# Optimization experiments

Hardware: AMD Instinct MI355X
Metric: run time of the kernel (lower is better)

The kernel has to match this reference:

```python
import jax, jax.numpy as jnp
import numpy as np

N, E = 40000, 640000
D, H, DK = 128, 8, 16   # out_dim, n_heads, d_k = D // H
T, R = 3, 4             # num node types, num relation types


def setup_inputs() -> dict:
    key = jax.random.key(0)
    ks = jax.random.split(key, 16)
    glorot = lambda k, shape, fan: jax.random.normal(k, shape, jnp.float32) * np.sqrt(2.0 / fan)
    inp = {
        'node_inp': jax.random.normal(ks[0], (N, D), jnp.float32),
        'node_type': jax.random.randint(ks[1], (N,), 0, T),
        'edge_index': jax.random.randint(ks[2], (2, E), 0, N),
        'edge_type': jax.random.randint(ks[3], (E,), 0, R),
        'node_position': jax.random.randint(ks[4], (N,), 0, N),
        # per-node-type Linear weights, stored [T, in, out] (y = x @ W + b)
        'Kw': glorot(ks[5], (T, D, D), 2 * D), 'Kb': jnp.zeros((T, D), jnp.float32),
        'Qw': glorot(ks[6], (T, D, D), 2 * D), 'Qb': jnp.zeros((T, D), jnp.float32),
        'Vw': glorot(ks[7], (T, D, D), 2 * D), 'Vb': jnp.zeros((T, D), jnp.float32),
        'Aw': glorot(ks[8], (T, D, D), 2 * D), 'Ab': jnp.zeros((T, D), jnp.float32),
        'relation_pri': jnp.ones((T, R, T, H), jnp.float32),
        'relation_att': glorot(ks[9], (R, H, DK, DK), 2 * DK),
        'relation_msg': glorot(ks[10], (R, H, DK, DK), 2 * DK),
        'relation_s2u': glorot(ks[11], (D, D), 2 * D),
        'skip': jnp.ones((T,), jnp.float32),
    }
    return inp


def reference(node_inp, node_type, edge_index, edge_type, node_position,
              Kw, Kb, Qw, Qb, Vw, Vb, Aw, Ab,
              relation_pri, relation_att, relation_msg, relation_s2u, skip):
    n = node_inp.shape[0]
    src, tgt = edge_index[0], edge_index[1]  # j (source), i (target)
    ar = jnp.arange(n)

    # per-type K/Q/V projections for every node: [T, N, D], then select own type
    k_all = jnp.einsum('nd,tdo->tno', node_inp, Kw) + Kb[:, None, :]
    q_all = jnp.einsum('nd,tdo->tno', node_inp, Qw) + Qb[:, None, :]
    v_all = jnp.einsum('nd,tdo->tno', node_inp, Vw) + Vb[:, None, :]
    k_node = k_all[node_type, ar]
    q_node = q_all[node_type, ar]
    v_node = v_all[node_type, ar]

    k_j = k_node[src].reshape(-1, H, DK)
    v_j = v_node[src].reshape(-1, H, DK)
    q_i = q_node[tgt].reshape(-1, H, DK)

    # per-relation attention / message transforms (select per edge relation)
    k_t = jnp.zeros_like(k_j)
    v_t = jnp.zeros_like(v_j)
    for r in range(R):
        sel = (edge_type == r)[:, None, None]
        k_t = jnp.where(sel, jnp.einsum('ehd,hdf->ehf', k_j, relation_att[r]), k_t)
        v_t = jnp.where(sel, jnp.einsum('ehd,hdf->ehf', v_j, relation_msg[r]), v_t)

    st, tt = node_type[src], node_type[tgt]
    pri = relation_pri[tt, edge_type, st]                       # [E, H]
    att_raw = (q_i * k_t).sum(-1) * pri / np.sqrt(DK)           # [E, H]

    # scatter-softmax over edges sharing the same target node
    m = jax.ops.segment_max(att_raw, tgt, num_segments=n)
    m = jnp.where(jnp.isfinite(m), m, 0.0)
    ex = jnp.exp(att_raw - m[tgt])
    den = jax.ops.segment_sum(ex, tgt, num_segments=n)
    att = ex / (den[tgt] + 1e-16)

    msg = (v_t * att[:, :, None]).reshape(-1, D)
    aggr = jax.ops.segment_sum(msg, tgt, num_segments=n)        # scatter-add

    # speaker information: edges with edge_type==0, message from target rep to source index
    sp_in = v_all[1][tgt]                                       # v_linears[1](node_inp[edge_index_i])
    sp_msg = sp_in @ relation_s2u                               # [E, D]
    drop_idx = jnp.where(edge_type == 0, src, n)                # out-of-range -> dropped
    speaker_info = jnp.zeros((n, D), node_inp.dtype).at[drop_idx].set(sp_msg, mode='drop')

    aggr = jax.nn.gelu(aggr + speaker_info, approximate=False)

    # target-specific aggregation with per-type learnable skip (dropout=eval identity)
    a_all = jnp.einsum('no,tof->tnf', aggr, Aw) + Ab[:, None, :]
    a_node = a_all[node_type, ar]
    alpha = jax.nn.sigmoid(skip)[node_type][:, None]
    return a_node * alpha + node_inp * (1.0 - alpha)
```

## Files before the change

kernel.cpp:

```cpp
#include <hip/hip_runtime.h>
#include <hip/hip_bf16.h>
#include <math.h>

#define ND 128
#define NH 8
#define DKK 16
#define NT 3
#define NR 4
#define NB 8
#define NMAT 12
#define SCB 4096

typedef unsigned short ushort_t;
typedef __bf16 bf16_t;
typedef bf16_t bf16x8 __attribute__((ext_vector_type(8)));
typedef float f32x4 __attribute__((ext_vector_type(4)));

__device__ __forceinline__ float bf2f(unsigned short u) {
    union { unsigned int i; float f; } v; v.i = ((unsigned int)u) << 16; return v.f;
}
__device__ __forceinline__ unsigned short f2bf(float f) {
    union { float f; unsigned int i; } v; v.f = f;
    unsigned int x = v.i;
    unsigned int lsb = (x >> 16) & 1u;
    x += 0x7fffu + lsb;
    return (unsigned short)(x >> 16);
}
__device__ __forceinline__ unsigned int pk2(float a, float b) {
    return (unsigned int)f2bf(a) | ((unsigned int)f2bf(b) << 16);
}
__device__ __forceinline__ void load_bf8(const ushort_t* p, float* o) {
    uint4 u = *reinterpret_cast<const uint4*>(p);
    o[0]=bf2f(u.x & 0xffff); o[1]=bf2f(u.x >> 16);
    o[2]=bf2f(u.y & 0xffff); o[3]=bf2f(u.y >> 16);
    o[4]=bf2f(u.z & 0xffff); o[5]=bf2f(u.z >> 16);
    o[6]=bf2f(u.w & 0xffff); o[7]=bf2f(u.w >> 16);
}
__device__ __forceinline__ void cvt8(uint4 u, float* o) {
    o[0]=bf2f(u.x & 0xffff); o[1]=bf2f(u.x >> 16);
    o[2]=bf2f(u.y & 0xffff); o[3]=bf2f(u.y >> 16);
    o[4]=bf2f(u.z & 0xffff); o[5]=bf2f(u.z >> 16);
    o[6]=bf2f(u.w & 0xffff); o[7]=bf2f(u.w >> 16);
}
__device__ __forceinline__ bf16x8 as_bf16x8(uint4 u) {
    union { uint4 u; bf16x8 v; } c; c.u = u; return c.v;
}


__global__ void k_zero(int n, int* offs, int* winner) {
    int i = blockIdx.x * 256 + threadIdx.x;
    if (i < n) { offs[i] = 0; winner[i] = -1; }
}

__global__ void k_count(int e, const int* src, const int* tgt, const int* etype,
                        int* offs, int* winner, int* rank) {
    int i = blockIdx.x * 256 + threadIdx.x;
    if (i < e) {
        rank[i] = atomicAdd(&offs[tgt[i]], 1);
        if (etype[i] == 0) atomicMax(&winner[src[i]], i);
    }
}


__global__ void k_scanA(int n, const int* offs, const int* ntype, int* bsum4) {
    __shared__ int red[256];
    __shared__ int tr[256][3];
    int b = blockIdx.x, tid = threadIdx.x;
    int base = b * SCB + tid * 16;
    int s = 0, c0 = 0, c1 = 0, c2 = 0;
    #pragma unroll
    for (int i = 0; i < 16; i++) {
        int idx = base + i;
        if (idx < n) {
            s += offs[idx];
            int t = ntype[idx];
            c0 += (t == 0); c1 += (t == 1); c2 += (t == 2);
        }
    }
    red[tid] = s; tr[tid][0] = c0; tr[tid][1] = c1; tr[tid][2] = c2;
    __syncthreads();
    for (int d = 128; d > 0; d >>= 1) {
        if (tid < d) {
            red[tid] += red[tid + d];
            tr[tid][0] += tr[tid + d][0];
            tr[tid][1] += tr[tid + d][1];
            tr[tid][2] += tr[tid + d][2];
        }
        __syncthreads();
    }
    if (tid == 0) {
        bsum4[b * 4]     = red[0];
        bsum4[b * 4 + 1] = tr[0][0];
        bsum4[b * 4 + 2] = tr[0][1];
        bsum4[b * 4 + 3] = tr[0][2];
    }
}

__global__ void k_scanB(int nb, const int* bsum4, int* boff4, int* tcnt, int* tstart) {
    if (threadIdx.x == 0) {
        int run = 0, r0 = 0, r1 = 0, r2 = 0;
        for (int b = 0; b < nb; b++) {
            boff4[b * 4]     = run;
            boff4[b * 4 + 1] = r0;
            boff4[b * 4 + 2] = r1;
            boff4[b * 4 + 3] = r2;
            run += bsum4[b * 4];
            r0  += bsum4[b * 4 + 1];
            r1  += bsum4[b * 4 + 2];
            r2  += bsum4[b * 4 + 3];
        }
        tcnt[0] = r0; tcnt[1] = r1; tcnt[2] = r2;
        tstart[0] = 0; tstart[1] = r0; tstart[2] = r0 + r1;
    }
}

__global__ void k_scanC(int n, int* offs, const int* ntype, const int* boff4,
                        const int* tstart, int* order) {
    __shared__ int red[256];
    __shared__ int tr[256][3];
    int b = blockIdx.x, tid = threadIdx.x;
    int base = b * SCB + tid * 16;
    int v[16]; signed char ty[16];
    int s = 0, c0 = 0, c1 = 0, c2 = 0;
    #pragma unroll
    for (int i = 0; i < 16; i++) {
        int idx = base + i;
        v[i] = (idx < n) ? offs[idx] : 0;
        s += v[i];
        int t = (idx < n) ? ntype[idx] : -1;
        ty[i] = (signed char)t;
        c0 += (t == 0); c1 += (t == 1); c2 += (t == 2);
    }
    red[tid] = s; tr[tid][0] = c0; tr[tid][1] = c1; tr[tid][2] = c2;
    __syncthreads();
    for (int d = 1; d < 256; d <<= 1) {
        int vv = (tid >= d) ? red[tid - d] : 0;
        int w0 = (tid >= d) ? tr[tid - d][0] : 0;
        int w1 = (tid >= d) ? tr[tid - d][1] : 0;
        int w2 = (tid >= d) ? tr[tid - d][2] : 0;
        __syncthreads();
        red[tid] += vv; tr[tid][0] += w0; tr[tid][1] += w1; tr[tid][2] += w2;
        __syncthreads();
    }
    int run = boff4[b * 4] + red[tid] - s;
    int p0 = tstart[0] + boff4[b * 4 + 1] + tr[tid][0] - c0;
    int p1 = tstart[1] + boff4[b * 4 + 2] + tr[tid][1] - c1;
    int p2 = tstart[2] + boff4[b * 4 + 3] + tr[tid][2] - c2;
    #pragma unroll
    for (int i = 0; i < 16; i++) {
        int idx = base + i;
        if (idx < n) {
            offs[idx] = run; run += v[i];
            int t = ty[i];
            if (t == 0)      order[p0++] = idx;
            else if (t == 1) order[p1++] = idx;
            else             order[p2++] = idx;
        }
    }
    if (base <= n && n < base + 16) offs[n] = run;
}

__global__ void k_scatter(int e, const int* src, const int* tgt, const int* etype,
                          const int* ntype, const int* offs, const int* rank,
                          int* eord, int mode) {
    int i = blockIdx.x * 256 + threadIdx.x;
    if (i < e) {
        int p = offs[tgt[i]] + rank[i];
        if (mode) {
            int s = src[i];
            eord[p] = (s * NR + etype[i]) | (ntype[s] << 28);
        } else {
            eord[p] = i;
        }
    }
}


__global__ void k_pack(const float* Qw, const float* Qb, const float* Kw, const float* Kb,
                       const float* Vw, const float* Vb, const float* Aw, const float* Ab,
                       const float* s2u, const float* r_att, const float* r_msg,
                       ushort_t* Wall, float* bcat) {
    int blk = blockIdx.x;
    int kb = blk & 3;
    int c = (blk >> 2) & 7;
    int tm = blk >> 5;
    int m = tm % NMAT, t = tm / NMAT;
    int lane = threadIdx.x;
    int nn = c * 16 + (lane & 15);
    int quad = lane >> 4;
    int k0 = kb * 32 + quad * 8;
    ushort_t* dst = Wall + (size_t)blk * 512 + lane * 8;

    if (m == 0 || m == 5 || m == 10 || m == 11) {
        const float* W; const float* B;
        if (m == 0)       { W = Qw + (size_t)t * ND * ND; B = Qb + t * ND; }
        else if (m == 5)  { W = Vw + (size_t)ND * ND;     B = Vb + ND; }
        else if (m == 10) { W = Aw + (size_t)t * ND * ND; B = Ab + t * ND; }
        else              { W = s2u;                      B = nullptr; }
        #pragma unroll
        for (int j = 0; j < 8; j++) dst[j] = f2bf(W[(size_t)(k0 + j) * ND + nn]);
        if (kb == 0 && quad == 0)
            bcat[(t * NMAT + m) * ND + nn] = B ? B[nn] : 0.f;
    } else {
        int r = (m <= 4) ? (m - 1) : (m - 6);
        const float* W0 = (m <= 4) ? Kw : Vw;
        const float* B0 = (m <= 4) ? Kb : Vb;
        const float* Wr = (m <= 4) ? r_att : r_msg;
        int h = c, f = lane & 15;
        float wcol[16];
        #pragma unroll
        for (int jj = 0; jj < 16; jj++)
            wcol[jj] = Wr[(((size_t)r * NH + h) * DKK + jj) * DKK + f];
        #pragma unroll
        for (int j = 0; j < 8; j++) {
            const float* row = W0 + ((size_t)t * ND + (k0 + j)) * ND + h * DKK;
            float s = 0.f;
            #pragma unroll
            for (int jj = 0; jj < 16; jj++) s += row[jj] * wcol[jj];
            dst[j] = f2bf(s);
        }
        if (kb == 0 && quad == 0) {
            const float* brow = B0 + t * ND + h * DKK;
            float sb = 0.f;
            #pragma unroll
            for (int jj = 0; jj < 16; jj++) sb += brow[jj] * wcol[jj];
            bcat[(t * NMAT + m) * ND + nn] = sb;
        }
    }
}

__global__ void __launch_bounds__(256) k_projm(
    int n, const float* x_in, const int* order,
    const int* tcnt, const int* tstart,
    const ushort_t* Wall, const float* bcat,
    int m0, int nm,
    ushort_t* out_qn, ushort_t* out_kt, ushort_t* out_v1, ushort_t* out_vt)
{
    __shared__ __align__(16) ushort_t xs[4096];
    __shared__ int nodes[32];
    int b = blockIdx.x;
    int nb0 = (tcnt[0] + 31) >> 5, nb1 = (tcnt[1] + 31) >> 5, nb2 = (tcnt[2] + 31) >> 5;
    int t, lb;
    if (b < nb0)                  { t = 0; lb = b; }
    else if (b < nb0 + nb1)       { t = 1; lb = b - nb0; }
    else if (b < nb0 + nb1 + nb2) { t = 2; lb = b - nb0 - nb1; }
    else return;
    int segoff = lb * 32;
    int cnt = min(32, tcnt[t] - segoff);
    int segbase = tstart[t] + segoff;
    int tid = threadIdx.x;
    if (tid < 32) nodes[tid] = (tid < cnt) ? order[segbase + tid] : -1;
    __syncthreads();
    {
        int row = tid >> 3;
        int d0 = (tid & 7) * 16;
        int rt = row >> 4, rl = row & 15;
        int kb = d0 >> 5, q0 = (d0 >> 3) & 3;
        uint4 c0, c1;
        if (row < cnt) {
            const float4* xp4 = (const float4*)(x_in + (size_t)nodes[row] * ND + d0);
            float4 a = xp4[0], b2 = xp4[1], c2 = xp4[2], d4 = xp4[3];
            c0.x = pk2(a.x, a.y);   c0.y = pk2(a.z, a.w);
            c0.z = pk2(b2.x, b2.y); c0.w = pk2(b2.z, b2.w);
            c1.x = pk2(c2.x, c2.y); c1.y = pk2(c2.z, c2.w);
            c1.z = pk2(d4.x, d4.y); c1.w = pk2(d4.z, d4.w);
        } else {
            c0.x = c0.y = c0.z = c0.w = 0u;
            c1 = c0;
        }
        *(uint4*)&xs[((rt * 4 + kb) * 64 + q0 * 16 + rl) * 8]       = c0;
        *(uint4*)&xs[((rt * 4 + kb) * 64 + (q0 + 1) * 16 + rl) * 8] = c1;
    }
    __syncthreads();

    int w = tid >> 6, lane = tid & 63;
    int rt = w & 1;
    bf16x8 afr[4];
    #pragma unroll
    for (int kb = 0; kb < 4; kb++)
        afr[kb] = as_bf16x8(*(const uint4*)&xs[((rt * 4 + kb) * 64 + lane) * 8]);
    int nct = nm * 8;
    for (int ct = (w >> 1); ct < nct; ct += 2) {
        int m = m0 + (ct >> 3), c = ct & 7;
        const uint4* bp = (const uint4*)(Wall + ((((size_t)t * NMAT + m) * 8 + c) * 4) * 512);
        f32x4 acc = {0.f, 0.f, 0.f, 0.f};
        #pragma unroll
        for (int kb = 0; kb < 4; kb++) {
            bf16x8 bfr = as_bf16x8(bp[kb * 64 + lane]);
            acc = __builtin_amdgcn_mfma_f32_16x16x32_bf16(afr[kb], bfr, acc, 0, 0, 0);
        }
        int col = c * 16 + (lane & 15);
        float bias = bcat[(t * NMAT + m) * ND + col];
        int rbase = rt * 16 + (lane >> 4) * 4;
        #pragma unroll
        for (int r = 0; r < 4; r++) {
            int grow = rbase + r;
            if (grow >= cnt) continue;
            int node = nodes[grow];
            ushort_t val = f2bf(acc[r] + bias);
            if (m == 0)       out_qn[(size_t)node * ND + col] = val;
            else if (m <= 4)  out_kt[((size_t)node * NR + (m - 1)) * ND + col] = val;
            else if (m == 5)  out_v1[(size_t)node * ND + col] = val;
            else              out_vt[((size_t)node * NR + (m - 6)) * ND + col] = val;
        }
    }
}

__global__ void __launch_bounds__(256) k_projall(
    int n, const float* x_in, const int* order,
    const int* tcnt, const int* tstart,
    const ushort_t* Wall, const float* bcat,
    ushort_t* out_qn, ushort_t* out_kt, ushort_t* out_v1, ushort_t* out_vt)
{
    __shared__ __align__(16) ushort_t xs[4096];
    __shared__ int nodes[32];
    int b = blockIdx.x;
    int nb0 = (tcnt[0] + 31) >> 5, nb1 = (tcnt[1] + 31) >> 5, nb2 = (tcnt[2] + 31) >> 5;
    int t, lb;
    if (b < nb0)                  { t = 0; lb = b; }
    else if (b < nb0 + nb1)       { t = 1; lb = b - nb0; }
    else if (b < nb0 + nb1 + nb2) { t = 2; lb = b - nb0 - nb1; }
    else return;
    int segoff = lb * 32;
    int cnt = min(32, tcnt[t] - segoff);
    int segbase = tstart[t] + segoff;
    int tid = threadIdx.x;
    if (tid < 32) nodes[tid] = (tid < cnt) ? order[segbase + tid] : -1;
    __syncthreads();
    {
        int row = tid >> 3;
        int d0 = (tid & 7) * 16;
        int rt = row >> 4, rl = row & 15;
        int kb = d0 >> 5, q0 = (d0 >> 3) & 3;
        uint4 c0, c1;
        if (row < cnt) {
            const float4* xp4 = (const float4*)(x_in + (size_t)nodes[row] * ND + d0);
            float4 a = xp4[0], b2 = xp4[1], c2 = xp4[2], d4 = xp4[3];
            c0.x = pk2(a.x, a.y);   c0.y = pk2(a.z, a.w);
            c0.z = pk2(b2.x, b2.y); c0.w = pk2(b2.z, b2.w);
            c1.x = pk2(c2.x, c2.y); c1.y = pk2(c2.z, c2.w);
            c1.z = pk2(d4.x, d4.y); c1.w = pk2(d4.z, d4.w);
        } else {
            c0.x = c0.y = c0.z = c0.w = 0u;
            c1 = c0;
        }
        *(uint4*)&xs[((rt * 4 + kb) * 64 + q0 * 16 + rl) * 8]       = c0;
        *(uint4*)&xs[((rt * 4 + kb) * 64 + (q0 + 1) * 16 + rl) * 8] = c1;
    }
    __syncthreads();

    int w = tid >> 6, lane = tid & 63;
    int rt = w & 1;
    bf16x8 afr[4];
    #pragma unroll
    for (int kb = 0; kb < 4; kb++)
        afr[kb] = as_bf16x8(*(const uint4*)&xs[((rt * 4 + kb) * 64 + lane) * 8]);
    for (int ct = (w >> 1); ct < 80; ct += 2) {
        int m = ct >> 3, c = ct & 7;
        const uint4* bp = (const uint4*)(Wall + ((((size_t)t * NMAT + m) * 8 + c) * 4) * 512);
        f32x4 acc = {0.f, 0.f, 0.f, 0.f};
        #pragma unroll
        for (int kb = 0; kb < 4; kb++) {
            bf16x8 bfr = as_bf16x8(bp[kb * 64 + lane]);
            acc = __builtin_amdgcn_mfma_f32_16x16x32_bf16(afr[kb], bfr, acc, 0, 0, 0);
        }
        int col = c * 16 + (lane & 15);
        float bias = bcat[(t * NMAT + m) * ND + col];
        int rbase = rt * 16 + (lane >> 4) * 4;
        #pragma unroll
        for (int r = 0; r < 4; r++) {
            int grow = rbase + r;
            if (grow >= cnt) continue;
            int node = nodes[grow];
            ushort_t val = f2bf(acc[r] + bias);
            if (m == 0)       out_qn[(size_t)node * ND + col] = val;
            else if (m <= 4)  out_kt[((size_t)node * NR + (m - 1)) * ND + col] = val;
            else if (m == 5)  out_v1[(size_t)node * ND + col] = val;
            else              out_vt[((size_t)node * NR + (m - 6)) * ND + col] = val;
        }
    }
}

__global__ void __launch_bounds__(256) k_flash(
    int n, const int* off, const int* srp, const int* ntype,
    const ushort_t* qn, const ushort_t* kt, const ushort_t* vt,
    const float* r_pri, float* aggr)
{
    int wv = threadIdx.x >> 6, lane = threadIdx.x & 63;
    int i = blockIdx.x * 4 + wv;
    if (i >= n) return;
    int h = lane & 7, slot = lane >> 3;
    int hA = lane >> 3;
    int tt = ntype[i];
    float qf[16];
    load_bf8(qn + (size_t)i * ND + h * DKK, qf);
    load_bf8(qn + (size_t)i * ND + h * DKK + 8, qf + 8);
    const float* prib = r_pri + (size_t)(tt * NR * NT) * NH + h;
    int d0 = off[i], d1 = off[i + 1];
    float m = -3.0e38f, den = 0.f;
    float acc0 = 0.f, acc1 = 0.f;
    int sp_c = 0; bool live_c = false;
    uint4 ka_c, kb_c;
    ka_c.x = ka_c.y = ka_c.z = ka_c.w = 0u; kb_c = ka_c;
    if (d0 < d1) {
        int p = d0 + slot;
        live_c = (p < d1);
        sp_c = live_c ? srp[p] : 0;
        const uint4* kp = (const uint4*)(kt + (size_t)(sp_c & 0x0fffffff) * ND + h * DKK);
        ka_c = kp[0]; kb_c = kp[1];
    }
    for (int p0 = d0; p0 < d1; p0 += 8) {
        int np0 = p0 + 8;
        int sp_n = 0; bool live_n = false;
        uint4 ka_n, kb_n;
        ka_n.x = ka_n.y = ka_n.z = ka_n.w = 0u; kb_n = ka_n;
        if (np0 < d1) {
            int p = np0 + slot;
            live_n = (p < d1);
            sp_n = live_n ? srp[p] : 0;
            const uint4* kp = (const uint4*)(kt + (size_t)(sp_n & 0x0fffffff) * ND + h * DKK);
            ka_n = kp[0]; kb_n = kp[1];
        }
        int sr = sp_c & 0x0fffffff;
        int st = ((unsigned int)sp_c) >> 28;
        int r = sr & (NR - 1);
        float kf[16];
        cvt8(ka_c, kf); cvt8(kb_c, kf + 8);
        float a = 0.f;
        #pragma unroll
        for (int f = 0; f < 16; f++) a += qf[f] * kf[f];
        float pri = prib[(r * NT + st) * NH];
        float logit = fminf(fmaxf(a * pri * 0.25f, -1.0e4f), 1.0e4f);
        if (!live_c) logit = -3.0e38f;
        int nlive = min(d1 - p0, 8);
        unsigned int u[8];
        #pragma unroll
        for (int s = 0; s < 8; s++) {
            int srb = __shfl(sr, s * 8 + hA, 64);
            u[s] = (s < nlive) ? *reinterpret_cast<const unsigned int*>(
                        vt + (size_t)srb * ND + lane * 2) : 0u;
        }
        float cm = logit;
        #pragma unroll
        for (int d = 8; d < 64; d <<= 1) cm = fmaxf(cm, __shfl_xor(cm, d, 64));
        float mnew = fmaxf(m, cm);
        float w = live_c ? expf(logit - mnew) : 0.f;
        float ws = w;
        #pragma unroll
        for (int d = 8; d < 64; d <<= 1) ws += __shfl_xor(ws, d, 64);
        float scale = expf(m - mnew);
        den = den * scale + ws;
        m = mnew;
        float scaleA = __shfl(scale, hA, 64);
        acc0 *= scaleA; acc1 *= scaleA;
        #pragma unroll
        for (int s = 0; s < 8; s++) {
            if (s < nlive) {
                float wb = __shfl(w, s * 8 + hA, 64);
                acc0 += wb * bf2f(u[s] & 0xffff);
                acc1 += wb * bf2f(u[s] >> 16);
            }
        }
        sp_c = sp_n; live_c = live_n; ka_c = ka_n; kb_c = kb_n;
    }
    float denA = __shfl(den, hA, 64);
    float inv = 1.f / (denA + 1e-16f);
    float2 o; o.x = acc0 * inv; o.y = acc1 * inv;
    *reinterpret_cast<float2*>(aggr + (size_t)i * ND + lane * 2) = o;
}

__global__ void __launch_bounds__(256) k_sfinal(
    int n, const float* x_in, const int* order, const int* tcnt, const int* tstart,
    const int* winner, const int* tgt, const ushort_t* v1b,
    const ushort_t* Wall, const float* bcat, const float* skip,
    const float* aggr, float* out)
{
    __shared__ __align__(16) float xf[32 * 132];
    __shared__ __align__(16) ushort_t xs[4096];
    __shared__ int nodes[32];
    __shared__ int wsrc[32];
    int b = blockIdx.x;
    int nb0 = (tcnt[0] + 31) >> 5, nb1 = (tcnt[1] + 31) >> 5, nb2 = (tcnt[2] + 31) >> 5;
    int t, lb;
    if (b < nb0)                  { t = 0; lb = b; }
    else if (b < nb0 + nb1)       { t = 1; lb = b - nb0; }
    else if (b < nb0 + nb1 + nb2) { t = 2; lb = b - nb0 - nb1; }
    else return;
    int segoff = lb * 32;
    int cnt = min(32, tcnt[t] - segoff);
    int segbase = tstart[t] + segoff;
    int tid = threadIdx.x;
    if (tid < 32) {
        int nd = (tid < cnt) ? order[segbase + tid] : -1;
        nodes[tid] = nd;
        int wi = (nd >= 0) ? winner[nd] : -1;
        wsrc[tid] = (wi >= 0) ? tgt[wi] : -1;
    }
    __syncthreads();
    {
        int row = tid >> 3;
        int d0 = (tid & 7) * 16;
        int rt = row >> 4, rl = row & 15;
        int kb = d0 >> 5, q0 = (d0 >> 3) & 3;
        uint4 c0, c1;
        int s = (row < cnt) ? wsrc[row] : -1;
        if (s >= 0) {
            const uint4* vp = (const uint4*)(v1b + (size_t)s * ND + d0);
            c0 = vp[0]; c1 = vp[1];
        } else { c0.x = c0.y = c0.z = c0.w = 0u; c1 = c0; }
        *(uint4*)&xs[((rt * 4 + kb) * 64 + q0 * 16 + rl) * 8]       = c0;
        *(uint4*)&xs[((rt * 4 + kb) * 64 + (q0 + 1) * 16 + rl) * 8] = c1;
    }
    __syncthreads();
    int w = tid >> 6, lane = tid & 63;
    int rt = w & 1;
    {
        bf16x8 afr[4];
        #pragma unroll
        for (int kb = 0; kb < 4; kb++)
            afr[kb] = as_bf16x8(*(const uint4*)&xs[((rt * 4 + kb) * 64 + lane) * 8]);
        for (int ct = (w >> 1); ct < 8; ct += 2) {
            const uint4* bp = (const uint4*)(Wall + (((size_t)11 * 8 + ct) * 4) * 512);
            f32x4 acc = {0.f, 0.f, 0.f, 0.f};
            #pragma unroll
            for (int kb = 0; kb < 4; kb++) {
                bf16x8 bfr = as_bf16x8(bp[kb * 64 + lane]);
                acc = __builtin_amdgcn_mfma_f32_16x16x32_bf16(afr[kb], bfr, acc, 0, 0, 0);
            }
            int col = ct * 16 + (lane & 15);
            int rbase = rt * 16 + (lane >> 4) * 4;
            #pragma unroll
            for (int r = 0; r < 4; r++) {
                int grow = rbase + r;
                if (grow >= cnt) continue;
                int node = nodes[grow];
                float g = aggr[(size_t)node * ND + col] + acc[r];
                g = 0.5f * g * (1.f + erff(g * 0.70710678118f));
                xf[grow * 132 + col] = g;
            }
        }
    }
    __syncthreads();
    {
        int row = tid >> 3;
        int d0 = (tid & 7) * 16;
        int rt2 = row >> 4, rl = row & 15;
        int kb = d0 >> 5, q0 = (d0 >> 3) & 3;
        uint4 c0, c1;
        if (row < cnt) {
            const float4* xp4 = (const float4*)(xf + row * 132 + d0);
            float4 a = xp4[0], b2 = xp4[1], c2 = xp4[2], d4 = xp4[3];
            c0.x = pk2(a.x, a.y);   c0.y = pk2(a.z, a.w);
            c0.z = pk2(b2.x, b2.y); c0.w = pk2(b2.z, b2.w);
            c1.x = pk2(c2.x, c2.y); c1.y = pk2(c2.z, c2.w);
            c1.z = pk2(d4.x, d4.y); c1.w = pk2(d4.z, d4.w);
        } else {
            c0.x = c0.y = c0.z = c0.w = 0u;
            c1 = c0;
        }
        *(uint4*)&xs[((rt2 * 4 + kb) * 64 + q0 * 16 + rl) * 8]       = c0;
        *(uint4*)&xs[((rt2 * 4 + kb) * 64 + (q0 + 1) * 16 + rl) * 8] = c1;
    }
    __syncthreads();
    float alpha = 1.f / (1.f + expf(-skip[t]));
    {
        bf16x8 afr[4];
        #pragma unroll
        for (int kb = 0; kb < 4; kb++)
            afr[kb] = as_bf16x8(*(const uint4*)&xs[((rt * 4 + kb) * 64 + lane) * 8]);
        for (int ct = (w >> 1); ct < 8; ct += 2) {
            const uint4* bp = (const uint4*)(Wall + ((((size_t)t * NMAT + 10) * 8 + ct) * 4) * 512);
            f32x4 acc = {0.f, 0.f, 0.f, 0.f};
            #pragma unroll
            for (int kb = 0; kb < 4; kb++) {
                bf16x8 bfr = as_bf16x8(bp[kb * 64 + lane]);
                acc = __builtin_amdgcn_mfma_f32_16x16x32_bf16(afr[kb], bfr, acc, 0, 0, 0);
            }
            int col = ct * 16 + (lane & 15);
            float bias = bcat[(t * NMAT + 10) * ND + col];
            int rbase = rt * 16 + (lane >> 4) * 4;
            #pragma unroll
            for (int r = 0; r < 4; r++) {
                int grow = rbase + r;
                if (grow >= cnt) continue;
                int node = nodes[grow];
                float xin = x_in[(size_t)node * ND + col];
                out[(size_t)node * ND + col] = (acc[r] + bias) * alpha + xin * (1.f - alpha);
            }
        }
    }
}

__global__ void __launch_bounds__(256) k_attmd(
    int n, const int* off, const int* srp, const int* ntype,
    const ushort_t* qn, const ushort_t* kt, const float* r_pri,
    float* atts, ushort_t* mb, float* db)
{
    int wv = threadIdx.x >> 6, lane = threadIdx.x & 63;
    int i = blockIdx.x * 4 + wv;
    if (i >= n) return;
    int h = lane & 7, slot = lane >> 3;
    int tt = ntype[i];
    float qf[16];
    load_bf8(qn + (size_t)i * ND + h * DKK, qf);
    load_bf8(qn + (size_t)i * ND + h * DKK + 8, qf + 8);
    const float* prib = r_pri + (size_t)(tt * NR * NT) * NH + h;
    int d0 = off[i], d1 = off[i + 1];
    float m = -3.0e38f, den = 0.f;
    #pragma unroll 2
    for (int p0 = d0; p0 < d1; p0 += 8) {
        int p = p0 + slot;
        bool live = (p < d1);
        int sp = live ? srp[p] : 0;
        int sr = sp & 0x0fffffff;
        int st = ((unsigned int)sp) >> 28;
        int r = sr & (NR - 1);
        float kf[16];
        const ushort_t* kp = kt + (size_t)sr * ND + h * DKK;
        load_bf8(kp, kf);
        load_bf8(kp + 8, kf + 8);
        float a = 0.f;
        #pragma unroll
        for (int f = 0; f < 16; f++) a += qf[f] * kf[f];
        float pri = prib[(r * NT + st) * NH];
        float logit = fminf(fmaxf(a * pri * 0.25f, -1.0e4f), 1.0e4f);
        if (live) {
            atts[(size_t)p * NH + h] = logit;
            float mnew = fmaxf(m, logit);
            den = den * expf(m - mnew) + expf(logit - mnew);
            m = mnew;
        }
    }
    #pragma unroll
    for (int d = 8; d < 64; d <<= 1) {
        float mo = __shfl_xor(m, d, 64);
        float dn = __shfl_xor(den, d, 64);
        float mnew = fmaxf(m, mo);
        den = den * expf(m - mnew) + dn * expf(mo - mnew);
        m = mnew;
    }
    if (slot == 0) {
        ushort_t mh = (d1 > d0) ? f2bf(m) : (ushort_t)0;
        float dfin = (d1 > d0) ? den * expf(m - bf2f(mh)) : 0.f;
        mb[i * NH + h] = mh;
        db[i * NH + h] = dfin;
    }
}

__global__ void __launch_bounds__(256) k_aggr_fast(
    int n, const int* off, const int* srp, const ushort_t* vt, const float* atts,
    const ushort_t* mb, const float* db, float* aggr)
{
    int wv = threadIdx.x >> 6, lane = threadIdx.x & 63;
    int i = blockIdx.x * 4 + wv;
    if (i >= n) return;
    int h = lane >> 3;
    float mref = bf2f(mb[i * NH + h]);
    float inv = 1.f / (db[i * NH + h] + 1e-16f);
    int d0 = off[i], d1 = off[i + 1];
    float acc0 = 0.f, acc1 = 0.f;
    #pragma unroll 4
    for (int p = d0; p < d1; p++) {
        int sr = srp[p] & 0x0fffffff;
        float w = expf(atts[(size_t)p * NH + h] - mref) * inv;
        unsigned int u = *reinterpret_cast<const unsigned int*>(
            vt + (size_t)sr * ND + lane * 2);
        acc0 += w * bf2f(u & 0xffff);
        acc1 += w * bf2f(u >> 16);
    }
    float2 o; o.x = acc0; o.y = acc1;
    *reinterpret_cast<float2*>(aggr + (size_t)i * ND + lane * 2) = o;
}


__global__ void k_proj(int n, const float* x_in, const int* ntype, const int* order,
                       const float* Kw, const float* Kb,
                       const float* Qw, const float* Qb,
                       const float* Vw, const float* Vb,
                       ushort_t* kn, ushort_t* qn, ushort_t* vn, ushort_t* v1) {
    __shared__ float xs[NB][ND];
    __shared__ int nodes[NB];
    __shared__ int types[NB];
    int tid = threadIdx.x;
    int base = blockIdx.x * NB;
    int cnt = min(NB, n - base);
    if (tid < cnt) { int nd = order[base + tid]; nodes[tid] = nd; types[tid] = ntype[nd]; }
    __syncthreads();
    for (int j = 0; j < cnt; j++) xs[j][tid] = x_in[(size_t)nodes[j] * ND + tid];
    __syncthreads();
    bool uni = (types[0] == types[cnt - 1]);
    for (int m = 0; m < 4; m++) {
        const float *W, *B; ushort_t* out; int forced_t = -1;
        if (m == 0)      { W = Kw; B = Kb; out = kn; }
        else if (m == 1) { W = Qw; B = Qb; out = qn; }
        else if (m == 2) { W = Vw; B = Vb; out = vn; }
        else             { W = Vw; B = Vb; out = v1; forced_t = 1; }
        if (uni || forced_t >= 0) {
            int t = (forced_t >= 0) ? forced_t : types[0];
            float bias = B[t * ND + tid];
            float acc[NB];
            #pragma unroll
            for (int j = 0; j < NB; j++) acc[j] = bias;
            const float* Wp = W + (size_t)t * ND * ND + tid;
            for (int d = 0; d < ND; d++) {
                float w = Wp[(size_t)d * ND];
                #pragma unroll
                for (int j = 0; j < NB; j++) acc[j] += xs[j][d] * w;
            }
            for (int j = 0; j < cnt; j++) out[(size_t)nodes[j] * ND + tid] = f2bf(acc[j]);
        } else {
            for (int j = 0; j < cnt; j++) {
                int t = types[j];
                float acc = B[t * ND + tid];
                const float* Wp = W + (size_t)t * ND * ND + tid;
                for (int d = 0; d < ND; d++) acc += xs[j][d] * Wp[(size_t)d * ND];
                out[(size_t)nodes[j] * ND + tid] = f2bf(acc);
            }
        }
    }
}

__global__ void k_att(int e, const int* src, const int* tgt, const int* etype, const int* ntype,
                      const ushort_t* kn, const ushort_t* qn,
                      const float* r_att, const float* r_pri, float* att) {
    int id = blockIdx.x * 256 + threadIdx.x;
    if (id >= e * NH) return;
    int ee = id >> 3, h = id & 7;
    int s = src[ee], t = tgt[ee], r = etype[ee];
    float kf[16], qf[16];
    load_bf8(kn + (size_t)s * ND + h * DKK, kf);
    load_bf8(kn + (size_t)s * ND + h * DKK + 8, kf + 8);
    load_bf8(qn + (size_t)t * ND + h * DKK, qf);
    load_bf8(qn + (size_t)t * ND + h * DKK + 8, qf + 8);
    const float* W = r_att + (size_t)(r * NH + h) * DKK * DKK;
    float kt[16];
    #pragma unroll
    for (int f = 0; f < 16; f++) kt[f] = 0.f;
    #pragma unroll 4
    for (int d = 0; d < 16; d++) {
        float kd = kf[d];
        #pragma unroll
        for (int f = 0; f < 16; f++) kt[f] += kd * W[d * 16 + f];
    }
    float a = 0.f;
    #pragma unroll
    for (int f = 0; f < 16; f++) a += qf[f] * kt[f];
    int tt = ntype[t], st = ntype[s];
    float pri = r_pri[((tt * NR + r) * NT + st) * NH + h];
    float logit = a * pri * 0.25f;
    logit = fminf(fmaxf(logit, -1.0e4f), 1.0e4f);
    att[(size_t)ee * NH + h] = logit;
}

__global__ void k_mden(int n, const int* off, const int* sorted,
                       const float* att, ushort_t* mb, float* db) {
    int id = blockIdx.x * 256 + threadIdx.x;
    if (id >= n * NH) return;
    int i = id >> 3, h = id & 7;
    int d0 = off[i], d1 = off[i + 1];
    float m = -3.0e38f;
    for (int p = d0; p < d1; p++) m = fmaxf(m, att[(size_t)sorted[p] * NH + h]);
    ushort_t mh = (d1 > d0) ? f2bf(m) : (ushort_t)0;
    float mref = bf2f(mh);
    float den = 0.f;
    for (int p = d0; p < d1; p++) den += expf(att[(size_t)sorted[p] * NH + h] - mref);
    mb[id] = mh;
    db[id] = den;
}

__global__ void k_norm(int e, const int* tgt, const ushort_t* mb, const float* db, float* att) {
    int id = blockIdx.x * 256 + threadIdx.x;
    if (id >= e * NH) return;
    int ee = id >> 3, h = id & 7;
    int t = tgt[ee];
    float w = expf(att[id] - bf2f(mb[t * NH + h])) / (db[t * NH + h] + 1e-16f);
    att[id] = w;
}

__global__ void k_aggr(int n, const int* off, const int* sorted, const int* src, const int* etype,
                       const ushort_t* vn, const float* r_msg, const float* att, float* aggr) {
    int wv = threadIdx.x >> 6, lane = threadIdx.x & 63;
    int i = blockIdx.x * 4 + wv;
    if (i >= n) return;
    int h = lane >> 3, f0 = (lane & 7) * 2;
    int d0 = off[i], d1 = off[i + 1];
    float acc0 = 0.f, acc1 = 0.f;
    for (int p = d0; p < d1; p++) {
        int ee = sorted[p];
        int s = src[ee], r = etype[ee];
        float w = att[(size_t)ee * NH + h];
        float vj[16];
        load_bf8(vn + (size_t)s * ND + h * DKK, vj);
        load_bf8(vn + (size_t)s * ND + h * DKK + 8, vj + 8);
        const float* Wm = r_msg + (size_t)(r * NH + h) * DKK * DKK + f0;
        float a0 = 0.f, a1 = 0.f;
        #pragma unroll
        for (int d = 0; d < 16; d++) {
            a0 += vj[d] * Wm[d * 16];
            a1 += vj[d] * Wm[d * 16 + 1];
        }
        acc0 += w * a0; acc1 += w * a1;
    }
    aggr[(size_t)i * ND + h * DKK + f0]     = acc0;
    aggr[(size_t)i * ND + h * DKK + f0 + 1] = acc1;
}

__global__ void k_spk(int n, const int* winner, const int* tgt, const ushort_t* v1,
                      const float* s2u, float* aggr) {
    __shared__ float xs[NB][ND];
    __shared__ int wn[NB];
    int tid = threadIdx.x;
    int base = blockIdx.x * NB;
    int cnt = min(NB, n - base);
    if (tid < cnt) wn[tid] = winner[base + tid];
    __syncthreads();
    for (int j = 0; j < cnt; j++) {
        int w = wn[j];
        xs[j][tid] = (w >= 0) ? bf2f(v1[(size_t)tgt[w] * ND + tid]) : 0.f;
    }
    __syncthreads();
    float acc[NB];
    #pragma unroll
    for (int j = 0; j < NB; j++) acc[j] = 0.f;
    const float* Wp = s2u + tid;
    for (int d = 0; d < ND; d++) {
        float w = Wp[(size_t)d * ND];
        #pragma unroll
        for (int j = 0; j < NB; j++) acc[j] += xs[j][d] * w;
    }
    for (int j = 0; j < cnt; j++) {
        size_t idx = (size_t)(base + j) * ND + tid;
        float g = aggr[idx] + acc[j];
        g = 0.5f * g * (1.f + erff(g * 0.70710678118f));
        aggr[idx] = g;
    }
}

__global__ void k_final(int n, const float* x_in, const int* ntype, const int* order,
                        const float* Aw, const float* Ab, const float* skip,
                        const float* aggr, float* out) {
    __shared__ float xs[NB][ND];
    __shared__ int nodes[NB];
    __shared__ int types[NB];
    int tid = threadIdx.x;
    int base = blockIdx.x * NB;
    int cnt = min(NB, n - base);
    if (tid < cnt) { int nd = order[base + tid]; nodes[tid] = nd; types[tid] = ntype[nd]; }
    __syncthreads();
    for (int j = 0; j < cnt; j++) xs[j][tid] = aggr[(size_t)nodes[j] * ND + tid];
    __syncthreads();
    bool uni = (types[0] == types[cnt - 1]);
    if (uni) {
        int t = types[0];
        float bias = Ab[t * ND + tid];
        float acc[NB];
        #pragma unroll
        for (int j = 0; j < NB; j++) acc[j] = bias;
        const float* Wp = Aw + (size_t)t * ND * ND + tid;
        for (int d = 0; d < ND; d++) {
            float w = Wp[(size_t)d * ND];
            #pragma unroll
            for (int j = 0; j < NB; j++) acc[j] += xs[j][d] * w;
        }
        float alpha = 1.f / (1.f + expf(-skip[t]));
        for (int j = 0; j < cnt; j++) {
            float xin = x_in[(size_t)nodes[j] * ND + tid];
            out[(size_t)nodes[j] * ND + tid] = acc[j] * alpha + xin * (1.f - alpha);
        }
    } else {
        for (int j = 0; j < cnt; j++) {
            int t = types[j];
            float acc = Ab[t * ND + tid];
            const float* Wp = Aw + (size_t)t * ND * ND + tid;
            for (int d = 0; d < ND; d++) acc += xs[j][d] * Wp[(size_t)d * ND];
            float alpha = 1.f / (1.f + expf(-skip[t]));
            float xin = x_in[(size_t)nodes[j] * ND + tid];
            out[(size_t)nodes[j] * ND + tid] = acc * alpha + xin * (1.f - alpha);
        }
    }
}

extern "C" void kernel_launch(void* const* d_in, const int* in_sizes, int n_in,
                              void* d_out, int out_size, void* d_ws, size_t ws_size,
                              hipStream_t stream) {
    const float* node_inp = (const float*)d_in[0];
    const int* node_type  = (const int*)d_in[1];
    const int* edge_index = (const int*)d_in[2];
    const int* edge_type  = (const int*)d_in[3];
    const float* Kw = (const float*)d_in[5];
    const float* Kb = (const float*)d_in[6];
    const float* Qw = (const float*)d_in[7];
    const float* Qb = (const float*)d_in[8];
    const float* Vw = (const float*)d_in[9];
    const float* Vb = (const float*)d_in[10];
    const float* Aw = (const float*)d_in[11];
    const float* Ab = (const float*)d_in[12];
    const float* r_pri = (const float*)d_in[13];
    const float* r_att = (const float*)d_in[14];
    const float* r_msg = (const float*)d_in[15];
    const float* s2u   = (const float*)d_in[16];
    const float* skip  = (const float*)d_in[17];

    int n = in_sizes[1];
    int e = in_sizes[3];
    const int* srcp = edge_index;
    const int* tgtp = edge_index + e;

    char* wsp = (char*)d_ws;
    size_t woff = 0;
    auto alloc = [&](size_t b) { void* p = wsp + woff; woff += (b + 255) & ~(size_t)255; return p; };

    int* offs     = (int*)alloc((size_t)(n + 1) * 4);
    int* winner   = (int*)alloc((size_t)n * 4);
    int* order    = (int*)alloc((size_t)n * 4);
    int* tcnt     = (int*)alloc(16);
    int* tstart   = (int*)alloc(16);
    int* bsum4    = (int*)alloc(4096);
    int* boff4    = (int*)alloc(4096);
    int* eord     = (int*)alloc((size_t)e * 4);
    ushort_t* mb  = (ushort_t*)alloc((size_t)n * NH * 2);
    float* db     = (float*)alloc((size_t)n * NH * 4);
    ushort_t* v1b = (ushort_t*)alloc((size_t)n * ND * 2);
    float* att    = (float*)alloc((size_t)e * NH * 4);
    size_t commonEnd = woff;

    int* rank = (int*)att;

    woff = commonEnd;
    ushort_t* WallB = (ushort_t*)alloc((size_t)NT * NMAT * 8 * 4 * 512 * 2);
    float* bcatB    = (float*)alloc((size_t)NT * NMAT * ND * 4);
    char* F         = (char*)alloc((size_t)n * 1536);
    size_t fastEnd = woff;

    woff = commonEnd;
    ushort_t* WallA = (ushort_t*)alloc((size_t)NT * NMAT * 8 * 4 * 512 * 2);
    float* bcatA    = (float*)alloc((size_t)NT * NMAT * ND * 4);
    ushort_t* qnA   = (ushort_t*)alloc((size_t)n * ND * 2);
    ushort_t* ktA   = (ushort_t*)alloc((size_t)n * NR * ND * 2);
    ushort_t* vtA   = (ushort_t*)alloc((size_t)n * NR * ND * 2);
    size_t tierAEnd = woff;
    float* aggrA = (float*)att;

    int gn = (n + 255) / 256;
    int ge = (e + 255) / 256;
    int nbscan = n / SCB + 1;
    int gproj = (n + 31) / 32 + NT;

    int tierA = (ws_size >= tierAEnd) && ((size_t)e * NH >= (size_t)n * ND);
    int fast  = (ws_size >= fastEnd);

    k_zero<<<gn, 256, 0, stream>>>(n, offs, winner);
    k_count<<<ge, 256, 0, stream>>>(e, srcp, tgtp, edge_type, offs, winner, rank);
    k_scanA<<<nbscan, 256, 0, stream>>>(n, offs, node_type, bsum4);
    k_scanB<<<1, 64, 0, stream>>>(nbscan, bsum4, boff4, tcnt, tstart);
    k_scanC<<<nbscan, 256, 0, stream>>>(n, offs, node_type, boff4, tstart, order);
    k_scatter<<<ge, 256, 0, stream>>>(e, srcp, tgtp, edge_type, node_type, offs, rank,
                                      eord, (tierA || fast) ? 1 : 0);

    if (tierA) {
        k_pack<<<NT * NMAT * 8 * 4, 64, 0, stream>>>(Qw, Qb, Kw, Kb, Vw, Vb, Aw, Ab,
                                                     s2u, r_att, r_msg, WallA, bcatA);
        k_projall<<<gproj, 256, 0, stream>>>(n, node_inp, order, tcnt, tstart, WallA, bcatA,
                                             qnA, ktA, v1b, vtA);
        k_flash<<<(n + 3) / 4, 256, 0, stream>>>(n, offs, eord, node_type,
                                                 qnA, ktA, vtA, r_pri, aggrA);
        k_sfinal<<<gproj, 256, 0, stream>>>(n, node_inp, order, tcnt, tstart,
                                            winner, tgtp, v1b, WallA, bcatA, skip,
                                            aggrA, (float*)d_out);
    } else if (fast) {
        ushort_t* qn  = (ushort_t*)F;
        ushort_t* kt  = (ushort_t*)(F + (size_t)n * 256);
        ushort_t* vt  = (ushort_t*)F;
        float* aggr   = (float*)(F + (size_t)n * 1024);

        k_pack<<<NT * NMAT * 8 * 4, 64, 0, stream>>>(Qw, Qb, Kw, Kb, Vw, Vb, Aw, Ab,
                                                     s2u, r_att, r_msg, WallB, bcatB);
        k_projm<<<gproj, 256, 0, stream>>>(n, node_inp, order, tcnt, tstart, WallB, bcatB,
                                           0, 6, qn, kt, v1b, (ushort_t*)nullptr);
        k_attmd<<<(n + 3) / 4, 256, 0, stream>>>(n, offs, eord, node_type,
                                                 qn, kt, r_pri, att, mb, db);
        k_projm<<<gproj, 256, 0, stream>>>(n, node_inp, order, tcnt, tstart, WallB, bcatB,
                                           6, 4, (ushort_t*)nullptr, (ushort_t*)nullptr,
                                           (ushort_t*)nullptr, vt);
        k_aggr_fast<<<(n + 3) / 4, 256, 0, stream>>>(n, offs, eord, vt, att, mb, db, aggr);
        k_sfinal<<<gproj, 256, 0, stream>>>(n, node_inp, order, tcnt, tstart,
                                            winner, tgtp, v1b, WallB, bcatB, skip,
                                            aggr, (float*)d_out);
    } else {
        woff = commonEnd;
        ushort_t* vn  = (ushort_t*)alloc((size_t)n * ND * 2);
        char* regA    = (char*)alloc((size_t)n * ND * 2 * 2);
        ushort_t* kn  = (ushort_t*)regA;
        ushort_t* qn  = (ushort_t*)(regA + (size_t)n * ND * 2);
        float* aggr   = (float*)regA;

        k_proj<<<(n + NB - 1) / NB, 128, 0, stream>>>(n, node_inp, node_type, order,
                                                      Kw, Kb, Qw, Qb, Vw, Vb, kn, qn, vn, v1b);
        k_att<<<(e * NH + 255) / 256, 256, 0, stream>>>(e, srcp, tgtp, edge_type, node_type,
                                                        kn, qn, r_att, r_pri, att);
        k_mden<<<(n * NH + 255) / 256, 256, 0, stream>>>(n, offs, eord, att, mb, db);
        k_norm<<<(e * NH + 255) / 256, 256, 0, stream>>>(e, tgtp, mb, db, att);
        k_aggr<<<(n + 3) / 4, 256, 0, stream>>>(n, offs, eord, srcp, edge_type, vn, r_msg, att, aggr);
        k_spk<<<(n + NB - 1) / NB, 128, 0, stream>>>(n, winner, tgtp, v1b, s2u, aggr);
        k_final<<<(n + NB - 1) / NB, 128, 0, stream>>>(n, node_inp, node_type, order,
                                                       Aw, Ab, skip, aggr, (float*)d_out);
    }
}
```

Baseline: 312.7 us.

## Apply relation message transform after aggregation instead of precomputing per-relation V

Rather than projecting V through each of the four relation_msg matrices per node (n×4×D output), the projection now writes a single per-type V, and the flash kernel keeps four per-relation accumulators. It then applies the relation_msg 16x16 transform once per node at the end using shuffles. This cuts projection MFMA work and the per-node V storage and gather traffic by a factor of four. In exchange the flash kernel gets more registers, a data-dependent branch per edge, and a 64-step shuffle-multiply epilogue that reads weights from global memory.

```diff
diff --git a/kernel.cpp b/kernel.cpp
--- a/kernel.cpp
+++ b/kernel.cpp
@@ -8,7 +8,7 @@
 #define NT 3
 #define NR 4
 #define NB 8
-#define NMAT 12
+#define NMAT 13
 #define SCB 4096
 
 typedef unsigned short ushort_t;
@@ -191,11 +191,12 @@
     int k0 = kb * 32 + quad * 8;
     ushort_t* dst = Wall + (size_t)blk * 512 + lane * 8;
 
-    if (m == 0 || m == 5 || m == 10 || m == 11) {
+    if (m == 0 || m == 5 || m == 10 || m == 11 || m == 12) {
         const float* W; const float* B;
         if (m == 0)       { W = Qw + (size_t)t * ND * ND; B = Qb + t * ND; }
         else if (m == 5)  { W = Vw + (size_t)ND * ND;     B = Vb + ND; }
         else if (m == 10) { W = Aw + (size_t)t * ND * ND; B = Ab + t * ND; }
+        else if (m == 12) { W = Vw + (size_t)t * ND * ND; B = Vb + t * ND; }
         else              { W = s2u;                      B = nullptr; }
         #pragma unroll
         for (int j = 0; j < 8; j++) dst[j] = f2bf(W[(size_t)(k0 + j) * ND + nn]);
@@ -310,7 +311,7 @@
     int n, const float* x_in, const int* order,
     const int* tcnt, const int* tstart,
     const ushort_t* Wall, const float* bcat,
-    ushort_t* out_qn, ushort_t* out_kt, ushort_t* out_v1, ushort_t* out_vt)
+    ushort_t* out_qn, ushort_t* out_kt, ushort_t* out_v1, ushort_t* out_vn)
 {
     __shared__ __align__(16) ushort_t xs[4096];
     __shared__ int nodes[32];
@@ -355,8 +356,9 @@
     #pragma unroll
     for (int kb = 0; kb < 4; kb++)
         afr[kb] = as_bf16x8(*(const uint4*)&xs[((rt * 4 + kb) * 64 + lane) * 8]);
-    for (int ct = (w >> 1); ct < 80; ct += 2) {
-        int m = ct >> 3, c = ct & 7;
+    for (int ci = (w >> 1); ci < 56; ci += 2) {
+        int m = (ci < 48) ? (ci >> 3) : 12;
+        int c = ci & 7;
         const uint4* bp = (const uint4*)(Wall + ((((size_t)t * NMAT + m) * 8 + c) * 4) * 512);
         f32x4 acc = {0.f, 0.f, 0.f, 0.f};
         #pragma unroll
@@ -376,15 +378,15 @@
             if (m == 0)       out_qn[(size_t)node * ND + col] = val;
             else if (m <= 4)  out_kt[((size_t)node * NR + (m - 1)) * ND + col] = val;
             else if (m == 5)  out_v1[(size_t)node * ND + col] = val;
-            else              out_vt[((size_t)node * NR + (m - 6)) * ND + col] = val;
+            else              out_vn[(size_t)node * ND + col] = val;
         }
     }
 }
 
 __global__ void __launch_bounds__(256) k_flash(
     int n, const int* off, const int* srp, const int* ntype,
-    const ushort_t* qn, const ushort_t* kt, const ushort_t* vt,
-    const float* r_pri, float* aggr)
+    const ushort_t* qn, const ushort_t* kt, const ushort_t* vn,
+    const float* r_pri, const float* r_msg, float* aggr)
 {
     int wv = threadIdx.x >> 6, lane = threadIdx.x & 63;
     int i = blockIdx.x * 4 + wv;
@@ -398,7 +400,8 @@
     const float* prib = r_pri + (size_t)(tt * NR * NT) * NH + h;
     int d0 = off[i], d1 = off[i + 1];
     float m = -3.0e38f, den = 0.f;
-    float acc0 = 0.f, acc1 = 0.f;
+    float a00 = 0.f, a01 = 0.f, a02 = 0.f, a03 = 0.f;
+    float a10 = 0.f, a11 = 0.f, a12 = 0.f, a13 = 0.f;
     int sp_c = 0; bool live_c = false;
     uint4 ka_c, kb_c;
     ka_c.x = ka_c.y = ka_c.z = ka_c.w = 0u; kb_c = ka_c;
@@ -434,11 +437,13 @@
         if (!live_c) logit = -3.0e38f;
         int nlive = min(d1 - p0, 8);
         unsigned int u[8];
+        int rbv[8];
         #pragma unroll
         for (int s = 0; s < 8; s++) {
             int srb = __shfl(sr, s * 8 + hA, 64);
+            rbv[s] = srb & (NR - 1);
             u[s] = (s < nlive) ? *reinterpret_cast<const unsigned int*>(
-                        vt + (size_t)srb * ND + lane * 2) : 0u;
+                        vn + (size_t)(srb >> 2) * ND + lane * 2) : 0u;
         }
         float cm = logit;
         #pragma unroll
@@ -452,20 +457,41 @@
         den = den * scale + ws;
         m = mnew;
         float scaleA = __shfl(scale, hA, 64);
-        acc0 *= scaleA; acc1 *= scaleA;
+        a00 *= scaleA; a01 *= scaleA; a02 *= scaleA; a03 *= scaleA;
+        a10 *= scaleA; a11 *= scaleA; a12 *= scaleA; a13 *= scaleA;
         #pragma unroll
         for (int s = 0; s < 8; s++) {
             if (s < nlive) {
                 float wb = __shfl(w, s * 8 + hA, 64);
-                acc0 += wb * bf2f(u[s] & 0xffff);
-                acc1 += wb * bf2f(u[s] >> 16);
+                float v0 = wb * bf2f(u[s] & 0xffff);
+                float v1 = wb * bf2f(u[s] >> 16);
+                int rb = rbv[s];
+                if (rb == 0)      { a00 += v0; a10 += v1; }
+                else if (rb == 1) { a01 += v0; a11 += v1; }
+                else if (rb == 2) { a02 += v0; a12 += v1; }
+                else              { a03 += v0; a13 += v1; }
             }
         }
         sp_c = sp_n; live_c = live_n; ka_c = ka_n; kb_c = kb_n;
     }
     float denA = __shfl(den, hA, 64);
     float inv = 1.f / (denA + 1e-16f);
-    float2 o; o.x = acc0 * inv; o.y = acc1 * inv;
+    int f0 = (lane & 7) * 2;
+    float o0 = 0.f, o1 = 0.f;
+    #pragma unroll
+    for (int r = 0; r < 4; r++) {
+        float ar0 = (r == 0) ? a00 : (r == 1) ? a01 : (r == 2) ? a02 : a03;
+        float ar1 = (r == 0) ? a10 : (r == 1) ? a11 : (r == 2) ? a12 : a13;
+        const float* Wm = r_msg + ((size_t)(r * NH + hA) * DKK) * DKK + f0;
+        #pragma unroll
+        for (int d = 0; d < 16; d++) {
+            int srcl = hA * 8 + (d >> 1);
+            float sd = __shfl((d & 1) ? ar1 : ar0, srcl, 64);
+            o0 += sd * Wm[d * DKK];
+            o1 += sd * Wm[d * DKK + 1];
+        }
+    }
+    float2 o; o.x = o0 * inv; o.y = o1 * inv;
     *reinterpret_cast<float2*>(aggr + (size_t)i * ND + lane * 2) = o;
 }
 
@@ -937,7 +963,7 @@
     float* bcatA    = (float*)alloc((size_t)NT * NMAT * ND * 4);
     ushort_t* qnA   = (ushort_t*)alloc((size_t)n * ND * 2);
     ushort_t* ktA   = (ushort_t*)alloc((size_t)n * NR * ND * 2);
-    ushort_t* vtA   = (ushort_t*)alloc((size_t)n * NR * ND * 2);
+    ushort_t* vnA   = (ushort_t*)alloc((size_t)n * ND * 2);
     size_t tierAEnd = woff;
     float* aggrA = (float*)att;
 
@@ -961,9 +987,9 @@
         k_pack<<<NT * NMAT * 8 * 4, 64, 0, stream>>>(Qw, Qb, Kw, Kb, Vw, Vb, Aw, Ab,
                                                      s2u, r_att, r_msg, WallA, bcatA);
         k_projall<<<gproj, 256, 0, stream>>>(n, node_inp, order, tcnt, tstart, WallA, bcatA,
-                                             qnA, ktA, v1b, vtA);
+                                             qnA, ktA, v1b, vnA);
         k_flash<<<(n + 3) / 4, 256, 0, stream>>>(n, offs, eord, node_type,
-                                                 qnA, ktA, vtA, r_pri, aggrA);
+                                                 qnA, ktA, vnA, r_pri, r_msg, aggrA);
         k_sfinal<<<gproj, 256, 0, stream>>>(n, node_inp, order, tcnt, tstart,
                                             winner, tgtp, v1b, WallA, bcatA, skip,
                                             aggrA, (float*)d_out);
```

Result: slower. 358.2 us (+14.5%).
